# Kernel tuning notes

Measured on AMD Instinct MI355X. Metric: run time of the kernel, lower is better.

The kernel has to match this reference:

```python
import jax, jax.numpy as jnp
import numpy as np

B, S, H, E, C, V = 512, 256, 768, 6, 10, 3


def setup_inputs() -> dict:
    key = jax.random.key(0)
    ks = jax.random.split(key, 16)

    def w(k, shape):
        fan_in = shape[-1]
        return jax.random.normal(k, shape, dtype=jnp.float32) / np.sqrt(fan_in)

    return {
        'x': jax.random.randint(ks[0], (B, S), 0, V, dtype=jnp.int64),
        'emb': w(ks[1], (V, E)),
        'W_fx': w(ks[2], (H, E)), 'W_fh': w(ks[3], (H, H)), 'b_f': w(ks[4], (H, 1)),
        'W_ix': w(ks[5], (H, E)), 'W_ih': w(ks[6], (H, H)), 'b_i': w(ks[7], (H, 1)),
        'W_ox': w(ks[8], (H, E)), 'W_oh': w(ks[9], (H, H)), 'b_o': w(ks[10], (H, 1)),
        'W_cx': w(ks[11], (H, E)), 'b_c': w(ks[12], (H, 1)),
        'W_ph': w(ks[13], (C, H)), 'b_p': w(ks[14], (C, 1)),
        'c_init': jax.random.normal(ks[15], (H, B), dtype=jnp.float32) / np.sqrt(B),
    }


def reference(x, emb, W_fx, W_fh, b_f, W_ix, W_ih, b_i, W_ox, W_oh, b_o,
              W_cx, b_c, W_ph, b_p, c_init):
    # Embed tokens: [B, S] -> [B, S, E] -> time-major [S, E, B]
    xe = jnp.transpose(emb[x], (1, 2, 0))
    xs = xe[: S - 1]  # loop runs seq_length - 1 steps

    def step(carry, x_t):
        c_prev, _ = carry  # c_prev: [H, B], x_t: [E, B]
        f_t = jax.nn.sigmoid(W_fx @ x_t + W_fh @ c_prev + b_f)
        i_t = jax.nn.sigmoid(W_ix @ x_t + W_ih @ c_prev + b_i)
        o_t = jax.nn.sigmoid(W_ox @ x_t + W_oh @ c_prev + b_o)
        c_t = jax.nn.sigmoid(W_cx @ x_t + b_c) * i_t + c_prev * f_t
        h_t = jnp.tanh(c_t) * o_t
        return (c_t, h_t), None

    h0 = jnp.zeros((H, B), dtype=c_init.dtype)
    (c_fin, h_fin), _ = jax.lax.scan(step, (c_init, h0), xs)
    p_t = W_ph @ h_fin + b_p  # [C, B]
    return jax.nn.log_softmax(p_t.T, axis=-1)  # [B, C]
```

## Files before the change

kernel.cpp:

```cpp
#include <hip/hip_runtime.h>


typedef _Float16 f16x8 __attribute__((ext_vector_type(8)));
typedef _Float16 f16x4 __attribute__((ext_vector_type(4)));
typedef float    f32x4 __attribute__((ext_vector_type(4)));

#define Hdim  768
#define Bdim  512
#define Sdim  256
#define NSTEP 255
#define Edim  6
#define NCls  10
#define NGRP  16
#define NRB   12
#define GC    32
#define HB    64
#define NKK   24
#define NK2   12
#define CSTR  776
#define XSTR  260
#define ZSTR2 17
#define PLANE (Bdim * Hdim)
#define SCL      4096.0f
#define SCL_INV  2.44140625e-4f

#define WP_FRAGS   (2 * NRB * 4 * NKK * 64)
#define WS_CBUF    0u
#define WS_HFIN    (2u * 2u * PLANE * 2u)
#define WS_BAR     (WS_HFIN + Bdim * Hdim * 4u)
#define WS_WPK     (WS_BAR + 4096u)
#define WS_BAR_BYTES (NGRP * 16u * 4u)

__device__ __forceinline__ float sigf(float z) { return 1.0f / (1.0f + __expf(-z)); }

__device__ __forceinline__ f32x4 mf(f16x8 a, f16x8 b, f32x4 c) {
    return __builtin_amdgcn_mfma_f32_16x16x32_f16(a, b, c, 0, 0, 0);
}

__device__ __forceinline__ void keepalive(f16x8& x) {
    asm volatile("" : "+v"(x));
}

__global__ void __launch_bounds__(256)
prep_w(const float* __restrict__ Wfh, const float* __restrict__ Wih,
       _Float16* __restrict__ wpk)
{
    const int fid  = blockIdx.x * 256 + threadIdx.x;
    const int lane = fid & 63;
    const int t1   = fid >> 6;
    const int kk   = t1 % NKK;
    const int gi   = t1 / NKK;
    const int sub  = gi & 3;
    const int t3   = gi >> 2;
    const int rb   = t3 % NRB;
    const int gate = t3 / NRB;
    const int q = lane >> 4, r = lane & 15;
    const int row = rb * 64 + sub * 16 + r;
    const int col = kk * 32 + q * 8;
    const float* src = (gate ? Wih : Wfh) + (size_t)row * Hdim + col;
    f16x8 hi, lo;
    #pragma unroll
    for (int j = 0; j < 8; ++j) {
        const float v = src[j];
        const _Float16 h = (_Float16)v;
        hi[j] = h;
        lo[j] = (_Float16)((v - (float)h) * SCL);
    }
    *(f16x8*)&wpk[(size_t)fid * 8] = hi;
    *(f16x8*)&wpk[((size_t)WP_FRAGS + fid) * 8] = lo;
}

__global__ void __launch_bounds__(512, 1)
lstm_persist(const int* __restrict__ xk, const float* __restrict__ emb,
             const float* __restrict__ Wfx, const float* __restrict__ bfv,
             const float* __restrict__ Wix, const float* __restrict__ biv,
             const float* __restrict__ Wox, const float* __restrict__ Woh,
             const float* __restrict__ bov,
             const float* __restrict__ Wcx, const float* __restrict__ bcv,
             const float* __restrict__ cinit,
             const _Float16* __restrict__ wpk,
             _Float16* __restrict__ cbuf, float* __restrict__ hfin,
             unsigned int* __restrict__ bar)
{
    __shared__ __align__(16) _Float16 ldsH[GC * CSTR];
    __shared__ __align__(16) _Float16 ldsM[GC * CSTR];
    __shared__ __align__(16) float    tbl[3 * HB * 4];
    __shared__ __align__(16) float    zredA[4 * 2 * 64 * 4];
    __shared__ __align__(16) float    zredB[4 * 2 * 64 * 4];
    __shared__ __align__(16) float    zbufPA[2 * HB * ZSTR2];
    __shared__ __align__(16) float    zbufPB[2 * HB * ZSTR2];
    __shared__ __align__(4)  unsigned char xtok[GC * XSTR];
    __shared__ int s_flag;

    const int tid  = threadIdx.x;
    const int w    = tid >> 6;
    const int lane = tid & 63;
    const int q    = lane >> 4;
    const int r    = lane & 15;
    const int kh   = w & 1;
    const int pr   = w >> 1;
    const int gt   = pr >> 1;
    const int rh   = pr & 1;
    const int subp = rh * 2 + kh;
    const int bid  = blockIdx.x;
    const int g    = bid & 15;
    const int rb   = bid >> 4;
    const int blkh0 = rb * HB;
    const int gc0   = g * GC;
    const int hq0   = blkh0 + subp * 16 + q * 4;

    if (tid == 0) s_flag = 0;
    __syncthreads();
    if (tid < 256) {
        if (xk[(size_t)gc0 * Sdim + 2 * tid + 1] != 0) s_flag = 1;
    }
    if (tid < 3 * HB) {
        const int v  = tid >> 6;
        const int hl = tid & 63;
        const int hg = blkh0 + hl;
        float pf = bfv[hg], pi = biv[hg], po = bov[hg], pc = bcv[hg];
        #pragma unroll
        for (int e = 0; e < Edim; ++e) {
            const float ev = emb[v * Edim + e];
            pf += Wfx[hg * Edim + e] * ev;
            pi += Wix[hg * Edim + e] * ev;
            po += Wox[hg * Edim + e] * ev;
            pc += Wcx[hg * Edim + e] * ev;
        }
        float* t = &tbl[(v * HB + hl) * 4];
        t[0] = pf; t[1] = pi; t[2] = po; t[3] = sigf(pc);
    }
    __syncthreads();
    const int is64 = (s_flag == 0);

    {
        const int col   = tid >> 4;
        const int sbase = (tid & 15) * 16;
        const size_t rowb = (size_t)(gc0 + col) * Sdim;
        for (int k2 = 0; k2 < 16; ++k2) {
            const int s0 = sbase + k2;
            const size_t idx = rowb + s0;
            xtok[col * XSTR + s0] = (unsigned char)xk[is64 ? (idx << 1) : idx];
        }
    }

    f16x8 whi[2][NK2], wlo[2][NK2];
    #pragma unroll
    for (int s2 = 0; s2 < 2; ++s2) {
        const int gis = (gt * NRB + rb) * 4 + (rh * 2 + s2);
        #pragma unroll
        for (int k2 = 0; k2 < NK2; ++k2) {
            const size_t fo = ((size_t)(gis * NKK + kh * NK2 + k2) * 64 + lane) * 8;
            whi[s2][k2] = *(const f16x8*)&wpk[fo];
            wlo[s2][k2] = *(const f16x8*)&wpk[(size_t)WP_FRAGS * 8 + fo];
        }
    }
    #pragma unroll
    for (int s2 = 0; s2 < 2; ++s2)
        #pragma unroll
        for (int k2 = 0; k2 < NK2; ++k2) {
            keepalive(whi[s2][k2]);
            keepalive(wlo[s2][k2]);
        }

    float cst[2][4];
    #pragma unroll
    for (int ct = 0; ct < 2; ++ct) {
        const int b = gc0 + ct * 16 + r;
        #pragma unroll
        for (int reg = 0; reg < 4; ++reg)
            cst[ct][reg] = cinit[(size_t)(hq0 + reg) * Bdim + b];
    }

    for (int i = 0; i < 48; ++i) {
        const int idx = tid + i * 512;
        const int col = idx & 31, k = idx >> 5;
        const float v = cinit[(size_t)k * Bdim + gc0 + col];
        const _Float16 h = (_Float16)v;
        ldsH[col * CSTR + k] = h;
        ldsM[col * CSTR + k] = (_Float16)((v - (float)h) * SCL);
    }

    __syncthreads();

#define MFMA_HALF(ROWOFF, AH0, AX0, AH1, AX1)                                  \
    {                                                                          \
        _Pragma("unroll")                                                      \
        for (int k2 = 0; k2 < NK2; ++k2) {                                     \
            const int lo = (kh * NK2 + k2) * 32 + q * 8;                       \
            const f16x8 bh = *(const f16x8*)&ldsH[((ROWOFF) + r) * CSTR + lo]; \
            const f16x8 bm = *(const f16x8*)&ldsM[((ROWOFF) + r) * CSTR + lo]; \
            AH0 = mf(whi[0][k2], bh, AH0);                                     \
            AX0 = mf(whi[0][k2], bm, AX0);                                     \
            AX0 = mf(wlo[0][k2], bh, AX0);                                     \
            AH1 = mf(whi[1][k2], bh, AH1);                                     \
            AX1 = mf(whi[1][k2], bm, AX1);                                     \
            AX1 = mf(wlo[1][k2], bh, AX1);                                     \
        }                                                                      \
    }

#define SEND_PART(ZRED, AH0, AX0, AH1, AX1)                                    \
    {                                                                          \
        f32x4* zr_ = (f32x4*)(ZRED);                                           \
        zr_[(w * 2 + 0) * 64 + lane] = kh ? AH0 : AH1;                         \
        zr_[(w * 2 + 1) * 64 + lane] = kh ? AX0 : AX1;                         \
    }

#define IPART(ZBUF, AH0, AX0, AH1, AX1)                                        \
    {                                                                          \
        float* zp_ = &(ZBUF)[kh * (HB * ZSTR2)];                               \
        _Pragma("unroll")                                                      \
        for (int s2 = 0; s2 < 2; ++s2) {                                       \
            const f32x4 h_ = s2 ? AH1 : AH0;                                   \
            const f32x4 x_ = s2 ? AX1 : AX0;                                   \
            _Pragma("unroll")                                                  \
            for (int reg = 0; reg < 4; ++reg) {                                \
                const int row_ = rh * 32 + s2 * 16 + q * 4 + reg;              \
                zp_[row_ * ZSTR2 + r] = h_[reg] + x_[reg] * SCL_INV;           \
            }                                                                  \
        }                                                                      \
    }

#define REDUCE_K(ZRED, KH_, KX_, ZF)                                           \
    {                                                                          \
        const f32x4* zr_ = (const f32x4*)(ZRED);                               \
        const int pw_ = w ^ 1;                                                 \
        const f32x4 pH_ = zr_[(pw_ * 2 + 0) * 64 + lane];                      \
        const f32x4 pX_ = zr_[(pw_ * 2 + 1) * 64 + lane];                      \
        _Pragma("unroll")                                                      \
        for (int reg = 0; reg < 4; ++reg)                                      \
            ZF[reg] = (KH_[reg] + pH_[reg]) + (KX_[reg] + pX_[reg]) * SCL_INV; \
    }

#define EPILOGUE_C(CT, ZF, ZBUF)                                               \
    {                                                                          \
        _Float16* cwH = cbuf + (size_t)(((s + 1) & 1) * 2) * PLANE;            \
        _Float16* cwM = cwH + PLANE;                                           \
        const int bl = (CT) * 16 + r;                                          \
        const int v  = xtok[bl * XSTR + s];                                    \
        const float* tb = &tbl[(v * HB + subp * 16 + q * 4) * 4];              \
        f16x4 cvh, cvm;                                                        \
        _Pragma("unroll")                                                      \
        for (int reg = 0; reg < 4; ++reg) {                                    \
            const int rowl = subp * 16 + q * 4 + reg;                          \
            const float zi = (ZBUF)[rowl * ZSTR2 + r]                          \
                           + (ZBUF)[HB * ZSTR2 + rowl * ZSTR2 + r];            \
            const float* tt = tb + reg * 4;                                    \
            const float fg = sigf(ZF[reg] + tt[0]);                            \
            const float ig = sigf(zi + tt[1]);                                 \
            const float cn = tt[3] * ig + cst[CT][reg] * fg;                   \
            cst[CT][reg] = cn;                                                 \
            const _Float16 ch = (_Float16)cn;                                  \
            cvh[reg] = ch;                                                     \
            cvm[reg] = (_Float16)((cn - (float)ch) * SCL);                     \
        }                                                                      \
        unsigned long long uh, um;                                             \
        __builtin_memcpy(&uh, &cvh, 8);                                        \
        __builtin_memcpy(&um, &cvm, 8);                                        \
        const size_t eo = (size_t)(gc0 + bl) * Hdim + hq0;                     \
        __hip_atomic_store((unsigned long long*)&cwH[eo], uh,                  \
                           __ATOMIC_RELAXED, __HIP_MEMORY_SCOPE_AGENT);        \
        __hip_atomic_store((unsigned long long*)&cwM[eo], um,                  \
                           __ATOMIC_RELAXED, __HIP_MEMORY_SCOPE_AGENT);        \
    }

#define SPIN(TGT)                                                              \
    {                                                                          \
        const unsigned tgt_ = (TGT);                                           \
        while (true) {                                                         \
            unsigned vv_ = tgt_;                                               \
            if (lane < NRB)                                                    \
                vv_ = __hip_atomic_load(&bar[g * 16 + lane],                   \
                                        __ATOMIC_RELAXED,                      \
                                        __HIP_MEMORY_SCOPE_AGENT);             \
            if (__all(vv_ >= tgt_)) break;                                     \
            __builtin_amdgcn_s_sleep(2);                                       \
        }                                                                      \
        asm volatile("" ::: "memory");                                         \
    }

#define LOAD_HALF(LCOL, JJ)                                                    \
    {                                                                          \
        const _Float16* crH = cbuf + (size_t)(((s + 1) & 1) * 2) * PLANE;      \
        const _Float16* crM = crH + PLANE;                                     \
        const size_t rowo = (size_t)(gc0 + (LCOL)) * Hdim;                     \
        unsigned long long th[12];                                             \
        _Pragma("unroll")                                                      \
        for (int i = 0; i < 12; ++i)                                           \
            th[i] = __hip_atomic_load(                                         \
                (unsigned long long*)&crH[rowo + ((JJ) + 16 * i) * 4],         \
                __ATOMIC_RELAXED, __HIP_MEMORY_SCOPE_AGENT);                   \
        _Pragma("unroll")                                                      \
        for (int i = 0; i < 12; ++i)                                           \
            *(unsigned long long*)&ldsH[(LCOL) * CSTR + ((JJ) + 16 * i) * 4] = th[i]; \
        unsigned long long tm[12];                                             \
        _Pragma("unroll")                                                      \
        for (int i = 0; i < 12; ++i)                                           \
            tm[i] = __hip_atomic_load(                                         \
                (unsigned long long*)&crM[rowo + ((JJ) + 16 * i) * 4],         \
                __ATOMIC_RELAXED, __HIP_MEMORY_SCOPE_AGENT);                   \
        _Pragma("unroll")                                                      \
        for (int i = 0; i < 12; ++i)                                           \
            *(unsigned long long*)&ldsM[(LCOL) * CSTR + ((JJ) + 16 * i) * 4] = tm[i]; \
    }

    for (int s = 0; s < NSTEP; ++s) {
        const bool last = (s == NSTEP - 1);

        f32x4 ah0 = {0,0,0,0}, ax0 = {0,0,0,0}, ah1 = {0,0,0,0}, ax1 = {0,0,0,0};
        MFMA_HALF(0, ah0, ax0, ah1, ax1);

        if (gt == 0) { SEND_PART(zredA, ah0, ax0, ah1, ax1); }
        else         { IPART(zbufPA, ah0, ax0, ah1, ax1); }

        __syncthreads();

        f32x4 bh0v = {0,0,0,0}, bx0v = {0,0,0,0}, bh1v = {0,0,0,0}, bx1v = {0,0,0,0};
        float zfA[4];
        if (gt == 0) {
            const f32x4 kHa = kh ? ah1 : ah0;
            const f32x4 kXa = kh ? ax1 : ax0;
            REDUCE_K(zredA, kHa, kXa, zfA);
            if (!last) EPILOGUE_C(0, zfA, zbufPA);
            MFMA_HALF(16, bh0v, bx0v, bh1v, bx1v);
            SEND_PART(zredB, bh0v, bx0v, bh1v, bx1v);
        } else {
            MFMA_HALF(16, bh0v, bx0v, bh1v, bx1v);
            IPART(zbufPB, bh0v, bx0v, bh1v, bx1v);
        }

        asm volatile("s_waitcnt vmcnt(0)" ::: "memory");
        __syncthreads();

        if (!last) {
            if (tid == 0)
                __hip_atomic_store(&bar[g * 16 + rb], (unsigned)(2 * s + 1),
                                   __ATOMIC_RELAXED, __HIP_MEMORY_SCOPE_AGENT);
            if (gt == 0) {
                const f32x4 kHb = kh ? bh1v : bh0v;
                const f32x4 kXb = kh ? bx1v : bx0v;
                float zfB[4];
                REDUCE_K(zredB, kHb, kXb, zfB);
                EPILOGUE_C(1, zfB, zbufPB);
            } else {
                SPIN((unsigned)(2 * s + 1));
                const int lt = tid - 256;
                LOAD_HALF(lt >> 4, lt & 15);
            }
            asm volatile("s_waitcnt vmcnt(0)" ::: "memory");
            __syncthreads();
            if (tid == 0)
                __hip_atomic_store(&bar[g * 16 + rb], (unsigned)(2 * s + 2),
                                   __ATOMIC_RELAXED, __HIP_MEMORY_SCOPE_AGENT);
            if (gt == 0) {
                SPIN((unsigned)(2 * s + 2));
                LOAD_HALF(16 + (tid >> 4), tid & 15);
            }
        } else {
            if (gt == 0) {
                const f32x4 kHb = kh ? bh1v : bh0v;
                const f32x4 kXb = kh ? bx1v : bx0v;
                float zfB[4];
                REDUCE_K(zredB, kHb, kXb, zfB);

                f32x4 o0h = {0,0,0,0}, o0x = {0,0,0,0}, o1h = {0,0,0,0}, o1x = {0,0,0,0};
                const int arow = blkh0 + subp * 16 + r;
                #pragma unroll
                for (int kk = 0; kk < NKK; ++kk) {
                    const float* wp = Woh + (size_t)arow * Hdim + kk * 32 + q * 8;
                    f16x8 who;
                    #pragma unroll
                    for (int j = 0; j < 8; ++j) who[j] = (_Float16)wp[j];
                    const int lo = kk * 32 + q * 8;
                    const f16x8 bh0 = *(const f16x8*)&ldsH[ r       * CSTR + lo];
                    const f16x8 bm0 = *(const f16x8*)&ldsM[ r       * CSTR + lo];
                    const f16x8 bh1 = *(const f16x8*)&ldsH[(16 + r) * CSTR + lo];
                    const f16x8 bm1 = *(const f16x8*)&ldsM[(16 + r) * CSTR + lo];
                    o0h = mf(who, bh0, o0h);  o0x = mf(who, bm0, o0x);
                    o1h = mf(who, bh1, o1h);  o1x = mf(who, bm1, o1x);
                }
                #pragma unroll
                for (int ct = 0; ct < 2; ++ct) {
                    const int bl = ct * 16 + r;
                    const int v  = xtok[bl * XSTR + s];
                    const float* tb = &tbl[(v * HB + subp * 16 + q * 4) * 4];
                    const f32x4 zoh = ct ? o1h : o0h;
                    const f32x4 zox = ct ? o1x : o0x;
                    const float* zfp = ct ? zfB : zfA;
                    const float* zbp = ct ? zbufPB : zbufPA;
                    f32x4 hv;
                    #pragma unroll
                    for (int reg = 0; reg < 4; ++reg) {
                        const int rowl = subp * 16 + q * 4 + reg;
                        const float zi = zbp[rowl * ZSTR2 + r]
                                       + zbp[HB * ZSTR2 + rowl * ZSTR2 + r];
                        const float zo = zoh[reg] + zox[reg] * SCL_INV;
                        const float* tt = tb + reg * 4;
                        const float fg = sigf(zfp[reg] + tt[0]);
                        const float ig = sigf(zi + tt[1]);
                        const float og = sigf(zo + tt[2]);
                        const float cn = tt[3] * ig + cst[ct][reg] * fg;
                        const float e  = __expf(-2.0f * fabsf(cn));
                        const float th = __builtin_copysignf((1.0f - e) / (1.0f + e), cn);
                        hv[reg] = th * og;
                    }
                    *(f32x4*)&hfin[(size_t)(gc0 + bl) * Hdim + hq0] = hv;
                }
            }
        }
    }
}

__global__ void __launch_bounds__(64)
proj_kernel(const float* __restrict__ hfin, const float* __restrict__ Wph,
            const float* __restrict__ bpv, float* __restrict__ out)
{
    const int b = blockIdx.x;
    const int lane = threadIdx.x;
    float acc[NCls];
    #pragma unroll
    for (int c = 0; c < NCls; ++c) acc[c] = 0.f;
    const float* hb = &hfin[(size_t)b * Hdim];
    for (int i = 0; i < Hdim / 64; ++i) {
        const float hv = hb[lane + i * 64];
        #pragma unroll
        for (int c = 0; c < NCls; ++c)
            acc[c] += Wph[c * Hdim + lane + i * 64] * hv;
    }
    #pragma unroll
    for (int c = 0; c < NCls; ++c) {
        float v = acc[c];
        #pragma unroll
        for (int off = 32; off > 0; off >>= 1)
            v += __shfl_xor(v, off, 64);
        acc[c] = v + bpv[c];
    }
    float m = acc[0];
    #pragma unroll
    for (int c = 1; c < NCls; ++c) m = fmaxf(m, acc[c]);
    float ssum = 0.f;
    #pragma unroll
    for (int c = 0; c < NCls; ++c) ssum += __expf(acc[c] - m);
    const float lse = m + __logf(ssum);
    if (lane < NCls) out[b * NCls + lane] = acc[lane] - lse;
}

extern "C" void kernel_launch(void* const* d_in, const int* in_sizes, int n_in,
                              void* d_out, int out_size, void* d_ws, size_t ws_size,
                              hipStream_t stream)
{
    const int*   xk    = (const int*)d_in[0];
    const float* emb   = (const float*)d_in[1];
    const float* Wfx   = (const float*)d_in[2];
    const float* Wfh   = (const float*)d_in[3];
    const float* bfv   = (const float*)d_in[4];
    const float* Wix   = (const float*)d_in[5];
    const float* Wih   = (const float*)d_in[6];
    const float* biv   = (const float*)d_in[7];
    const float* Wox   = (const float*)d_in[8];
    const float* Woh   = (const float*)d_in[9];
    const float* bov   = (const float*)d_in[10];
    const float* Wcx   = (const float*)d_in[11];
    const float* bcv   = (const float*)d_in[12];
    const float* Wph   = (const float*)d_in[13];
    const float* bpv   = (const float*)d_in[14];
    const float* cinit = (const float*)d_in[15];

    char* ws = (char*)d_ws;
    _Float16*     cbuf = (_Float16*)(ws + WS_CBUF);
    float*        hfin = (float*)(ws + WS_HFIN);
    unsigned int* bar  = (unsigned int*)(ws + WS_BAR);
    _Float16*     wpk  = (_Float16*)(ws + WS_WPK);

    hipMemsetAsync(bar, 0, WS_BAR_BYTES, stream);

    prep_w<<<dim3(WP_FRAGS / 256), dim3(256), 0, stream>>>(Wfh, Wih, wpk);

    lstm_persist<<<dim3(NGRP * NRB), dim3(512), 0, stream>>>(
        xk, emb, Wfx, bfv, Wix, biv, Wox, Woh, bov, Wcx, bcv,
        cinit, wpk, cbuf, hfin, bar);

    proj_kernel<<<dim3(Bdim), dim3(64), 0, stream>>>(hfin, Wph, bpv, (float*)d_out);
}
```

Before: 2.310 ms.

## Restructure LSTM step into two sequential column halves with per-half barriers

Replaces the interleaved two-half schedule, where each half had its own LDS reduction buffers and gt-split epilogues, with a loop over two column halves that reuse a single set of buffers. The inter-block barrier is split into per-half counters so that loading half 1 of step s can wait on a flag from a different point in the schedule. All 512 threads now cooperate on each 16-column reload. The change trims LDS usage and simplifies the schedule, but it adds block-wide __syncthreads calls and serializes work that the old split by thread group overlapped.

```diff
diff --git a/kernel.cpp b/kernel.cpp
--- a/kernel.cpp
+++ b/kernel.cpp
@@ -29,7 +29,7 @@
 #define WS_HFIN    (2u * 2u * PLANE * 2u)
 #define WS_BAR     (WS_HFIN + Bdim * Hdim * 4u)
 #define WS_WPK     (WS_BAR + 4096u)
-#define WS_BAR_BYTES (NGRP * 16u * 4u)
+#define WS_BAR_BYTES (NGRP * 2u * 16u * 4u)
 
 __device__ __forceinline__ float sigf(float z) { return 1.0f / (1.0f + __expf(-z)); }
 
@@ -85,10 +85,8 @@
     __shared__ __align__(16) _Float16 ldsH[GC * CSTR];
     __shared__ __align__(16) _Float16 ldsM[GC * CSTR];
     __shared__ __align__(16) float    tbl[3 * HB * 4];
-    __shared__ __align__(16) float    zredA[4 * 2 * 64 * 4];
-    __shared__ __align__(16) float    zredB[4 * 2 * 64 * 4];
-    __shared__ __align__(16) float    zbufPA[2 * HB * ZSTR2];
-    __shared__ __align__(16) float    zbufPB[2 * HB * ZSTR2];
+    __shared__ __align__(16) float    zred[4 * 2 * 64 * 4];
+    __shared__ __align__(16) float    zbufP[2 * HB * ZSTR2];
     __shared__ __align__(4)  unsigned char xtok[GC * XSTR];
     __shared__ int s_flag;
 
@@ -264,13 +262,13 @@
                            __ATOMIC_RELAXED, __HIP_MEMORY_SCOPE_AGENT);        \
     }
 
-#define SPIN(TGT)                                                              \
+#define SPIN(HALFB, TGT)                                                       \
     {                                                                          \
         const unsigned tgt_ = (TGT);                                           \
         while (true) {                                                         \
             unsigned vv_ = tgt_;                                               \
             if (lane < NRB)                                                    \
-                vv_ = __hip_atomic_load(&bar[g * 16 + lane],                   \
+                vv_ = __hip_atomic_load(&bar[(g * 2 + (HALFB)) * 16 + lane],   \
                                         __ATOMIC_RELAXED,                      \
                                         __HIP_MEMORY_SCOPE_AGENT);             \
             if (__all(vv_ >= tgt_)) break;                                     \
@@ -279,127 +277,86 @@
         asm volatile("" ::: "memory");                                         \
     }
 
-#define LOAD_HALF(LCOL, JJ)                                                    \
-    {                                                                          \
-        const _Float16* crH = cbuf + (size_t)(((s + 1) & 1) * 2) * PLANE;      \
+#define LOAD_HALF16(COL0, PAR)                                                 \
+    {                                                                          \
+        const _Float16* crH = cbuf + (size_t)((PAR) * 2) * PLANE;              \
         const _Float16* crM = crH + PLANE;                                     \
-        const size_t rowo = (size_t)(gc0 + (LCOL)) * Hdim;                     \
-        unsigned long long th[12];                                             \
-        _Pragma("unroll")                                                      \
-        for (int i = 0; i < 12; ++i)                                           \
-            th[i] = __hip_atomic_load(                                         \
-                (unsigned long long*)&crH[rowo + ((JJ) + 16 * i) * 4],         \
+        const int col_ = (COL0) + (tid >> 5);                                  \
+        const int j_   = tid & 31;                                             \
+        const size_t rowo = (size_t)(gc0 + col_) * Hdim;                       \
+        unsigned long long th_[6], tm_[6];                                     \
+        _Pragma("unroll")                                                      \
+        for (int i = 0; i < 6; ++i)                                            \
+            th_[i] = __hip_atomic_load(                                        \
+                (unsigned long long*)&crH[rowo + (j_ + 32 * i) * 4],           \
                 __ATOMIC_RELAXED, __HIP_MEMORY_SCOPE_AGENT);                   \
         _Pragma("unroll")                                                      \
-        for (int i = 0; i < 12; ++i)                                           \
-            *(unsigned long long*)&ldsH[(LCOL) * CSTR + ((JJ) + 16 * i) * 4] = th[i]; \
-        unsigned long long tm[12];                                             \
-        _Pragma("unroll")                                                      \
-        for (int i = 0; i < 12; ++i)                                           \
-            tm[i] = __hip_atomic_load(                                         \
-                (unsigned long long*)&crM[rowo + ((JJ) + 16 * i) * 4],         \
+        for (int i = 0; i < 6; ++i)                                            \
+            tm_[i] = __hip_atomic_load(                                        \
+                (unsigned long long*)&crM[rowo + (j_ + 32 * i) * 4],           \
                 __ATOMIC_RELAXED, __HIP_MEMORY_SCOPE_AGENT);                   \
         _Pragma("unroll")                                                      \
-        for (int i = 0; i < 12; ++i)                                           \
-            *(unsigned long long*)&ldsM[(LCOL) * CSTR + ((JJ) + 16 * i) * 4] = tm[i]; \
+        for (int i = 0; i < 6; ++i)                                            \
+            *(unsigned long long*)&ldsH[col_ * CSTR + (j_ + 32 * i) * 4] = th_[i]; \
+        _Pragma("unroll")                                                      \
+        for (int i = 0; i < 6; ++i)                                            \
+            *(unsigned long long*)&ldsM[col_ * CSTR + (j_ + 32 * i) * 4] = tm_[i]; \
     }
 
     for (int s = 0; s < NSTEP; ++s) {
         const bool last = (s == NSTEP - 1);
 
-        f32x4 ah0 = {0,0,0,0}, ax0 = {0,0,0,0}, ah1 = {0,0,0,0}, ax1 = {0,0,0,0};
-        MFMA_HALF(0, ah0, ax0, ah1, ax1);
-
-        if (gt == 0) { SEND_PART(zredA, ah0, ax0, ah1, ax1); }
-        else         { IPART(zbufPA, ah0, ax0, ah1, ax1); }
-
-        __syncthreads();
-
-        f32x4 bh0v = {0,0,0,0}, bx0v = {0,0,0,0}, bh1v = {0,0,0,0}, bx1v = {0,0,0,0};
-        float zfA[4];
-        if (gt == 0) {
-            const f32x4 kHa = kh ? ah1 : ah0;
-            const f32x4 kXa = kh ? ax1 : ax0;
-            REDUCE_K(zredA, kHa, kXa, zfA);
-            if (!last) EPILOGUE_C(0, zfA, zbufPA);
-            MFMA_HALF(16, bh0v, bx0v, bh1v, bx1v);
-            SEND_PART(zredB, bh0v, bx0v, bh1v, bx1v);
-        } else {
-            MFMA_HALF(16, bh0v, bx0v, bh1v, bx1v);
-            IPART(zbufPB, bh0v, bx0v, bh1v, bx1v);
-        }
-
-        asm volatile("s_waitcnt vmcnt(0)" ::: "memory");
-        __syncthreads();
-
-        if (!last) {
-            if (tid == 0)
-                __hip_atomic_store(&bar[g * 16 + rb], (unsigned)(2 * s + 1),
-                                   __ATOMIC_RELAXED, __HIP_MEMORY_SCOPE_AGENT);
+        #pragma unroll
+        for (int half = 0; half < 2; ++half) {
+            const int colofs = half * 16;
+
+            f32x4 ah0 = {0,0,0,0}, ax0 = {0,0,0,0};
+            f32x4 ah1 = {0,0,0,0}, ax1 = {0,0,0,0};
+            MFMA_HALF(colofs, ah0, ax0, ah1, ax1);
+
+            if (gt == 0) { SEND_PART(zred, ah0, ax0, ah1, ax1); }
+            else         { IPART(zbufP, ah0, ax0, ah1, ax1); }
+
+            __syncthreads();
+
             if (gt == 0) {
-                const f32x4 kHb = kh ? bh1v : bh0v;
-                const f32x4 kXb = kh ? bx1v : bx0v;
-                float zfB[4];
-                REDUCE_K(zredB, kHb, kXb, zfB);
-                EPILOGUE_C(1, zfB, zbufPB);
-            } else {
-                SPIN((unsigned)(2 * s + 1));
-                const int lt = tid - 256;
-                LOAD_HALF(lt >> 4, lt & 15);
-            }
-            asm volatile("s_waitcnt vmcnt(0)" ::: "memory");
-            __syncthreads();
-            if (tid == 0)
-                __hip_atomic_store(&bar[g * 16 + rb], (unsigned)(2 * s + 2),
-                                   __ATOMIC_RELAXED, __HIP_MEMORY_SCOPE_AGENT);
-            if (gt == 0) {
-                SPIN((unsigned)(2 * s + 2));
-                LOAD_HALF(16 + (tid >> 4), tid & 15);
-            }
-        } else {
-            if (gt == 0) {
-                const f32x4 kHb = kh ? bh1v : bh0v;
-                const f32x4 kXb = kh ? bx1v : bx0v;
-                float zfB[4];
-                REDUCE_K(zredB, kHb, kXb, zfB);
-
-                f32x4 o0h = {0,0,0,0}, o0x = {0,0,0,0}, o1h = {0,0,0,0}, o1x = {0,0,0,0};
-                const int arow = blkh0 + subp * 16 + r;
-                #pragma unroll
-                for (int kk = 0; kk < NKK; ++kk) {
-                    const float* wp = Woh + (size_t)arow * Hdim + kk * 32 + q * 8;
-                    f16x8 who;
+                const f32x4 kH = kh ? ah1 : ah0;
+                const f32x4 kX = kh ? ax1 : ax0;
+                float zf[4];
+                REDUCE_K(zred, kH, kX, zf);
+
+                if (!last) {
+                    EPILOGUE_C(half, zf, zbufP);
+                } else {
+                    f32x4 oh = {0,0,0,0}, ox = {0,0,0,0};
+                    const int arow = blkh0 + subp * 16 + r;
                     #pragma unroll
-                    for (int j = 0; j < 8; ++j) who[j] = (_Float16)wp[j];
-                    const int lo = kk * 32 + q * 8;
-                    const f16x8 bh0 = *(const f16x8*)&ldsH[ r       * CSTR + lo];
-                    const f16x8 bm0 = *(const f16x8*)&ldsM[ r       * CSTR + lo];
-                    const f16x8 bh1 = *(const f16x8*)&ldsH[(16 + r) * CSTR + lo];
-                    const f16x8 bm1 = *(const f16x8*)&ldsM[(16 + r) * CSTR + lo];
-                    o0h = mf(who, bh0, o0h);  o0x = mf(who, bm0, o0x);
-                    o1h = mf(who, bh1, o1h);  o1x = mf(who, bm1, o1x);
-                }
-                #pragma unroll
-                for (int ct = 0; ct < 2; ++ct) {
-                    const int bl = ct * 16 + r;
+                    for (int kk = 0; kk < NKK; ++kk) {
+                        const float* wp = Woh + (size_t)arow * Hdim + kk * 32 + q * 8;
+                        f16x8 who;
+                        #pragma unroll
+                        for (int j = 0; j < 8; ++j) who[j] = (_Float16)wp[j];
+                        const int lo = kk * 32 + q * 8;
+                        const f16x8 bh = *(const f16x8*)&ldsH[(colofs + r) * CSTR + lo];
+                        const f16x8 bm = *(const f16x8*)&ldsM[(colofs + r) * CSTR + lo];
+                        oh = mf(who, bh, oh);
+                        ox = mf(who, bm, ox);
+                    }
+                    const int bl = colofs + r;
                     const int v  = xtok[bl * XSTR + s];
                     const float* tb = &tbl[(v * HB + subp * 16 + q * 4) * 4];
-                    const f32x4 zoh = ct ? o1h : o0h;
-                    const f32x4 zox = ct ? o1x : o0x;
-                    const float* zfp = ct ? zfB : zfA;
-                    const float* zbp = ct ? zbufPB : zbufPA;
                     f32x4 hv;
                     #pragma unroll
                     for (int reg = 0; reg < 4; ++reg) {
                         const int rowl = subp * 16 + q * 4 + reg;
-                        const float zi = zbp[rowl * ZSTR2 + r]
-                                       + zbp[HB * ZSTR2 + rowl * ZSTR2 + r];
-                        const float zo = zoh[reg] + zox[reg] * SCL_INV;
+                        const float zi = zbufP[rowl * ZSTR2 + r]
+                                       + zbufP[HB * ZSTR2 + rowl * ZSTR2 + r];
+                        const float zo = oh[reg] + ox[reg] * SCL_INV;
                         const float* tt = tb + reg * 4;
-                        const float fg = sigf(zfp[reg] + tt[0]);
+                        const float fg = sigf(zf[reg] + tt[0]);
                         const float ig = sigf(zi + tt[1]);
                         const float og = sigf(zo + tt[2]);
-                        const float cn = tt[3] * ig + cst[ct][reg] * fg;
+                        const float cn = tt[3] * ig + cst[half][reg] * fg;
                         const float e  = __expf(-2.0f * fabsf(cn));
                         const float th = __builtin_copysignf((1.0f - e) / (1.0f + e), cn);
                         hv[reg] = th * og;
@@ -407,6 +364,28 @@
                     *(f32x4*)&hfin[(size_t)(gc0 + bl) * Hdim + hq0] = hv;
                 }
             }
+
+            asm volatile("s_waitcnt vmcnt(0)" ::: "memory");
+            __syncthreads();
+
+            if (half == 0) {
+                if (!last && tid == 0)
+                    __hip_atomic_store(&bar[(g * 2 + 0) * 16 + rb], (unsigned)(s + 1),
+                                       __ATOMIC_RELAXED, __HIP_MEMORY_SCOPE_AGENT);
+                if (s > 0) {
+                    SPIN(1, (unsigned)s);
+                    LOAD_HALF16(16, s & 1);
+                }
+            } else {
+                if (!last) {
+                    if (tid == 0)
+                        __hip_atomic_store(&bar[(g * 2 + 1) * 16 + rb], (unsigned)(s + 1),
+                                           __ATOMIC_RELAXED, __HIP_MEMORY_SCOPE_AGENT);
+                    SPIN(0, (unsigned)(s + 1));
+                    LOAD_HALF16(0, (s + 1) & 1);
+                }
+            }
+            __syncthreads();
         }
     }
 }
```

After: 2.336 ms. About the same (+1.2%).
